# Kernel optimization log

Measured on AMD Instinct MI355X. Metric: run time of the kernel, lower is better.

## Reference

```python
import jax, jax.numpy as jnp
import numpy as np

B, C, H, W = 16, 512, 32, 32
HID = 4 * C


def setup_inputs() -> dict:
    key = jax.random.key(0)
    k_x, k_w1, k_w2 = jax.random.split(key, 3)
    x = jax.random.normal(k_x, (B, C, H, W), dtype=jnp.float32)
    # 1x1 conv weights stored as [out, in] matrices (kernel_size=1)
    w1 = jax.random.normal(k_w1, (HID, C), dtype=jnp.float32) * (1.0 / np.sqrt(C))
    b1 = jnp.zeros((HID,), dtype=jnp.float32)
    w2 = jax.random.normal(k_w2, (C, HID), dtype=jnp.float32) * (1.0 / np.sqrt(HID))
    b2 = jnp.zeros((C,), dtype=jnp.float32)
    return {"x": x, "w1": w1, "b1": b1, "w2": w2, "b2": b2}


def reference(x, w1, b1, w2, b2):
    Bd, Cd, Hd, Wd = x.shape
    scale = Cd ** (-0.5)
    xf = x.reshape(Bd, Cd, Hd * Wd)          # [B, C, N]
    q = jnp.swapaxes(xf, -1, -2)              # [B, N, C]
    # full spatial self-attention: scores [B, N, N]
    attn = jax.nn.softmax(jnp.einsum('bnc,bcm->bnm', q, xf) * scale, axis=-1)
    out = jnp.einsum('bnm,bmc->bnc', attn, q)  # [B, N, C]
    # 1x1-conv FFN applied per spatial position
    h = jax.nn.relu(jnp.einsum('bnc,dc->bnd', out, w1) + b1)   # [B, N, 4C]
    y = jnp.einsum('bnd,cd->bnc', h, w2) + b2                  # [B, N, C]
    y = jnp.swapaxes(y, -1, -2).reshape(Bd, Cd, Hd, Wd)
    return y + x
```

## Files before the change

### kernel.cpp

```cpp
#include <hip/hip_runtime.h>

#define BATCH 16
#define CH    512
#define NSP   1024
#define HIDD  2048

typedef __bf16 bf16x8 __attribute__((ext_vector_type(8)));
typedef float floatx4 __attribute__((ext_vector_type(4)));

__device__ __forceinline__ float bf2f(unsigned short u) {
    union { unsigned int i; float f; } v; v.i = ((unsigned int)u) << 16; return v.f;
}
__device__ __forceinline__ unsigned short f2bf(float f) {
    union { float f; unsigned int i; } v; v.f = f;
    unsigned int i = v.i;
    return (unsigned short)((i + 0x7FFFu + ((i >> 16) & 1u)) >> 16);
}

__device__ __forceinline__ void gload16(const void* g, void* l) {
    __builtin_amdgcn_global_load_lds(
        (__attribute__((address_space(1))) unsigned int*)(g),
        (__attribute__((address_space(3))) unsigned int*)(l),
        16, 0, 0);
}
#define MEMFENCE asm volatile("" ::: "memory")

template<int EPI, int MAP, int DEPTH>
__global__ __launch_bounds__(256, (DEPTH == 2) ? 3 : 2)
void gemm_bt(const unsigned short* __restrict__ A,
             const unsigned short* __restrict__ Bm,
             void* __restrict__ Cout,
             int Nn, int K,
             long sAb, long sBb, long sCb,
             const float* __restrict__ bias, float scale,
             const float* __restrict__ resid,
             float* __restrict__ aux)
{
    constexpr int NBUF = DEPTH + 1;
    __shared__ unsigned short sA[NBUF][128 * 32];
    __shared__ unsigned short sB[NBUF][128 * 32];

    const int tid  = threadIdx.x;
    const int lane = tid & 63;
    const int w    = tid >> 6;
    const int quad = lane >> 4;
    const int l15  = lane & 15;
    const int mw   = (w >> 1) * 64;
    const int nw   = (w & 1) * 64;

    const int F = blockIdx.x;
    int m0, n0, b;
    if constexpr (MAP == 0) {
        const int xcd = F & 7, s = F >> 3;
        b = xcd + ((s >> 6) << 3);
        const int j = s & 63; m0 = (j >> 3) << 7; n0 = (j & 7) << 7;
    } else if constexpr (MAP == 1) {
        const int xcd = F & 7, s = F >> 3;
        b = xcd + ((s >> 5) << 3);
        const int j = s & 31; m0 = (j >> 2) << 7; n0 = (j & 3) << 7;
    } else if constexpr (MAP == 2) {
        b = 0; m0 = (F >> 4) << 7; n0 = (F & 15) << 7;
    } else {
        const int xcd = F & 7, s = F >> 3;
        b = 0; m0 = (s & 3) << 7; n0 = ((xcd << 4) + (s >> 2)) << 7;
    }

    A  += (size_t)b * sAb;
    Bm += (size_t)b * sBb;

    const int srow = lane >> 2;
    const int sg   = (lane & 3) ^ ((lane >> 3) & 3);
    const unsigned short* pA = A  + (size_t)(m0 + w * 32 + srow) * K + sg * 8;
    const unsigned short* pB = Bm + (size_t)(n0 + w * 32 + srow) * K + sg * 8;
    const size_t rowskip16 = (size_t)16 * K;
    const int woff = w * 1024;
    const int rslot = ((l15 >> 1) & 3);

    floatx4 acc[4][4];
#pragma unroll
    for (int i = 0; i < 4; i++)
#pragma unroll
        for (int j = 0; j < 4; j++) acc[i][j] = (floatx4){0.f, 0.f, 0.f, 0.f};

    const int nIter = K >> 5;
    const int kLast = K - 32;

#pragma unroll
    for (int d = 0; d < DEPTH; ++d) {
        unsigned short* dA = &sA[d][0] + woff;
        unsigned short* dB = &sB[d][0] + woff;
        gload16(pA + d * 32,             dA);
        gload16(pA + d * 32 + rowskip16, dA + 512);
        gload16(pB + d * 32,             dB);
        gload16(pB + d * 32 + rowskip16, dB + 512);
        MEMFENCE;
    }

    int bcur = 0, bpf = DEPTH;
    for (int it = 0; it < nIter; ++it) {
        if constexpr (DEPTH == 2)
            asm volatile("s_waitcnt vmcnt(4)\n\ts_barrier" ::: "memory");
        else
            asm volatile("s_waitcnt vmcnt(8)\n\ts_barrier" ::: "memory");

        const int kpf = (it + DEPTH) * 32 <= kLast ? (it + DEPTH) * 32 : kLast;
        unsigned short* dA = &sA[0][0] + bpf * 4096 + woff;
        unsigned short* dB = &sB[0][0] + bpf * 4096 + woff;
        gload16(pA + kpf,             dA);
        gload16(pA + kpf + rowskip16, dA + 512);
        gload16(pB + kpf,             dB);
        gload16(pB + kpf + rowskip16, dB + 512);
        MEMFENCE;

        const unsigned short* bufA = &sA[0][0] + bcur * 4096;
        const unsigned short* bufB = &sB[0][0] + bcur * 4096;
        bf16x8 af[4], bfr[4];
#pragma unroll
        for (int mi = 0; mi < 4; mi++)
            af[mi] = *(const bf16x8*)(bufA + (mw + mi * 16 + l15) * 32
                                      + (quad ^ rslot) * 8);
#pragma unroll
        for (int ni = 0; ni < 4; ni++)
            bfr[ni] = *(const bf16x8*)(bufB + (nw + ni * 16 + l15) * 32
                                       + (quad ^ rslot) * 8);
#pragma unroll
        for (int mi = 0; mi < 4; mi++)
#pragma unroll
            for (int ni = 0; ni < 4; ni++)
                acc[mi][ni] = __builtin_amdgcn_mfma_f32_16x16x32_bf16(
                    af[mi], bfr[ni], acc[mi][ni], 0, 0, 0);

        bcur = bcur == NBUF - 1 ? 0 : bcur + 1;
        bpf  = bpf  == NBUF - 1 ? 0 : bpf  + 1;
    }
    asm volatile("s_waitcnt vmcnt(0)" ::: "memory");

    if constexpr (EPI == 4) {
        float* Of = (float*)Cout;
#pragma unroll
        for (int mi = 0; mi < 4; mi++) {
#pragma unroll
            for (int r = 0; r < 4; r++) {
                const int c = m0 + mw + mi * 16 + quad * 4 + r;
                const float bv = bias[c];
#pragma unroll
                for (int ni = 0; ni < 4; ni++) {
                    const int j  = n0 + nw + ni * 16 + l15;
                    const int bb = j >> 10, ns = j & 1023;
                    const size_t a = (size_t)bb * CH * NSP + (size_t)c * NSP + ns;
                    Of[a] = acc[mi][ni][r] + bv + resid[a];
                }
            }
        }
    } else if constexpr (EPI == 5) {
#pragma unroll
        for (int mi = 0; mi < 4; mi++)
#pragma unroll
            for (int ni = 0; ni < 4; ni++)
#pragma unroll
                for (int r = 0; r < 4; r++)
                    acc[mi][ni][r] = __expf(acc[mi][ni][r] * scale);
        {
            const int chunk = (n0 + nw) >> 6;
            float* ps = aux + (size_t)b * NSP * 16;
#pragma unroll
            for (int mi = 0; mi < 4; mi++) {
#pragma unroll
                for (int r = 0; r < 4; r++) {
                    float s = acc[mi][0][r] + acc[mi][1][r]
                            + acc[mi][2][r] + acc[mi][3][r];
                    s += __shfl_xor(s, 1);
                    s += __shfl_xor(s, 2);
                    s += __shfl_xor(s, 4);
                    s += __shfl_xor(s, 8);
                    if (l15 == 0)
                        ps[(size_t)(m0 + mw + mi * 16 + quad * 4 + r) * 16
                           + chunk] = s;
                }
            }
        }
        unsigned short* Cb = (unsigned short*)Cout + (size_t)b * sCb;
#pragma unroll
        for (int mi = 0; mi < 4; mi++) {
#pragma unroll
            for (int r = 0; r < 4; r++) {
                const size_t rowoff =
                    (size_t)(m0 + mw + mi * 16 + quad * 4 + r) * Nn;
#pragma unroll
                for (int ni = 0; ni < 4; ni++)
                    Cb[rowoff + n0 + nw + ni * 16 + l15] =
                        f2bf(acc[mi][ni][r]);
            }
        }
    } else if constexpr (EPI == 6) {
        const float* invp = aux + (size_t)b * NSP;
        unsigned short* Cb = (unsigned short*)Cout + (size_t)b * sCb;
#pragma unroll
        for (int mi = 0; mi < 4; mi++) {
#pragma unroll
            for (int r = 0; r < 4; r++) {
                const int row = m0 + mw + mi * 16 + quad * 4 + r;
                const float iv = invp[row];
                const size_t rowoff = (size_t)row * Nn;
#pragma unroll
                for (int ni = 0; ni < 4; ni++)
                    Cb[rowoff + n0 + nw + ni * 16 + l15] =
                        f2bf(acc[mi][ni][r] * iv);
            }
        }
    } else {
        unsigned short* Cb = (unsigned short*)Cout + (size_t)b * sCb;
        float bv[4];
#pragma unroll
        for (int ni = 0; ni < 4; ni++) bv[ni] = bias[n0 + nw + ni * 16 + l15];
#pragma unroll
        for (int mi = 0; mi < 4; mi++) {
#pragma unroll
            for (int r = 0; r < 4; r++) {
                const size_t rowoff =
                    (size_t)(m0 + mw + mi * 16 + quad * 4 + r) * Nn;
#pragma unroll
                for (int ni = 0; ni < 4; ni++)
                    Cb[rowoff + n0 + nw + ni * 16 + l15] =
                        f2bf(fmaxf(acc[mi][ni][r] + bv[ni], 0.f));
            }
        }
    }
}

__global__ __launch_bounds__(256)
void rowsum_inv_kernel(const float* __restrict__ ps, float* __restrict__ inv)
{
    const int i = blockIdx.x * 256 + threadIdx.x;
    const float* p = ps + (size_t)i * 16;
    float s = 0.f;
#pragma unroll
    for (int k = 0; k < 16; k++) s += p[k];
    inv[i] = 1.0f / s;
}

__global__ __launch_bounds__(256)
void pack_x_kernel(const float* __restrict__ x,
                   unsigned short* __restrict__ Xbf,
                   unsigned short* __restrict__ XT)
{
    __shared__ float tile[32][33];
    const int tx = threadIdx.x, ty = threadIdx.y;
    const int n0 = blockIdx.x * 32, c0 = blockIdx.y * 32, b = blockIdx.z;
    const size_t base = (size_t)b * CH * NSP;
#pragma unroll
    for (int i = ty; i < 32; i += 8) {
        float v = x[base + (size_t)(c0 + i) * NSP + n0 + tx];
        tile[i][tx] = v;
        Xbf[base + (size_t)(c0 + i) * NSP + n0 + tx] = f2bf(v);
    }
    __syncthreads();
    const size_t tbase = (size_t)b * NSP * CH;
#pragma unroll
    for (int i = ty; i < 32; i += 8)
        XT[tbase + (size_t)(n0 + i) * CH + c0 + tx] = f2bf(tile[tx][i]);
}

__global__ __launch_bounds__(256)
void cast_bf16_kernel(const float* __restrict__ src,
                      unsigned short* __restrict__ dst, int n)
{
    int i = blockIdx.x * 256 + threadIdx.x;
    if (i < n) dst[i] = f2bf(src[i]);
}

extern "C" void kernel_launch(void* const* d_in, const int* in_sizes, int n_in,
                              void* d_out, int out_size, void* d_ws, size_t ws_size,
                              hipStream_t stream)
{
    const float* x  = (const float*)d_in[0];
    const float* w1 = (const float*)d_in[1];
    const float* b1 = (const float*)d_in[2];
    const float* w2 = (const float*)d_in[3];
    const float* b2 = (const float*)d_in[4];
    float* out = (float*)d_out;

    char* ws = (char*)d_ws;
    unsigned short* Xbf = (unsigned short*)ws; ws += (size_t)BATCH * CH * NSP * 2;
    unsigned short* XT  = (unsigned short*)ws; ws += (size_t)BATCH * NSP * CH * 2;
    unsigned short* W1b = (unsigned short*)ws; ws += (size_t)HIDD * CH * 2;
    unsigned short* W2b = (unsigned short*)ws; ws += (size_t)CH * HIDD * 2;
    unsigned short* P   = (unsigned short*)ws; ws += (size_t)BATCH * NSP * NSP * 2;
    unsigned short* O   = (unsigned short*)ws; ws += (size_t)BATCH * NSP * CH * 2;
    unsigned short* Hb  = (unsigned short*)ws; ws += (size_t)BATCH * NSP * HIDD * 2;
    float*          Ps  = (float*)ws;          ws += (size_t)BATCH * NSP * 16 * 4;
    float*          Inv = (float*)ws;          ws += (size_t)BATCH * NSP * 4;

    const dim3 blk(256);

    pack_x_kernel<<<dim3(NSP / 32, CH / 32, BATCH), dim3(32, 8), 0, stream>>>(x, Xbf, XT);
    cast_bf16_kernel<<<dim3((HIDD * CH) / 256), blk, 0, stream>>>(w1, W1b, HIDD * CH);
    cast_bf16_kernel<<<dim3((CH * HIDD) / 256), blk, 0, stream>>>(w2, W2b, CH * HIDD);

    gemm_bt<5, 0, 2><<<dim3(1024), blk, 0, stream>>>(
        XT, XT, P, NSP, CH,
        (long)NSP * CH, (long)NSP * CH, (long)NSP * NSP, nullptr,
        0.04419417382415922f, nullptr, Ps);

    rowsum_inv_kernel<<<dim3(BATCH * NSP / 256), blk, 0, stream>>>(Ps, Inv);

    gemm_bt<6, 1, 2><<<dim3(512), blk, 0, stream>>>(
        P, Xbf, O, CH, NSP,
        (long)NSP * NSP, (long)CH * NSP, (long)NSP * CH, nullptr, 1.f,
        nullptr, Inv);

    gemm_bt<2, 2, 3><<<dim3(2048), blk, 0, stream>>>(
        O, W1b, Hb, HIDD, CH, 0, 0, 0, b1, 1.f, nullptr, nullptr);

    gemm_bt<4, 3, 3><<<dim3(512), blk, 0, stream>>>(
        W2b, Hb, out, BATCH * NSP, HIDD, 0, 0, 0, b2, 1.f, x, nullptr);
}
```

Measured before the change: 277.8 us.

## Exploit score matrix symmetry: compute upper-triangle tiles and mirror-write transposes

The X^T X score GEMM is symmetric, so the grid is reduced to upper-triangular 128x128 tiles per batch (36 per batch) and each off-diagonal tile also writes its transposed copy and the matching partial row sums. This cuts the matmul work for the score stage nearly in half at the cost of a second, transposed store pass and an uneven tile mapping. The FFN1 GEMM pipeline depth is also lowered from 3 to 2. It relies on the exponent of a symmetric score remaining symmetric, which holds here because the stabilisation is not row-dependent.

```diff
diff --git a/kernel.cpp b/kernel.cpp
--- a/kernel.cpp
+++ b/kernel.cpp
@@ -50,19 +50,22 @@
 
     const int F = blockIdx.x;
     int m0, n0, b;
-    if constexpr (MAP == 0) {
-        const int xcd = F & 7, s = F >> 3;
-        b = xcd + ((s >> 6) << 3);
-        const int j = s & 63; m0 = (j >> 3) << 7; n0 = (j & 7) << 7;
-    } else if constexpr (MAP == 1) {
+    if constexpr (MAP == 1) {
         const int xcd = F & 7, s = F >> 3;
         b = xcd + ((s >> 5) << 3);
         const int j = s & 31; m0 = (j >> 2) << 7; n0 = (j & 3) << 7;
     } else if constexpr (MAP == 2) {
         b = 0; m0 = (F >> 4) << 7; n0 = (F & 15) << 7;
-    } else {
+    } else if constexpr (MAP == 3) {
         const int xcd = F & 7, s = F >> 3;
         b = 0; m0 = (s & 3) << 7; n0 = ((xcd << 4) + (s >> 2)) << 7;
+    } else {
+        const int xcd = F & 7; int s = F >> 3;
+        b = xcd + ((s >= 36) ? 8 : 0);
+        if (s >= 36) s -= 36;
+        int tm = 0;
+        while (s >= 8 - tm) { s -= 8 - tm; tm++; }
+        m0 = tm << 7; n0 = (tm + s) << 7;
     }
 
     A  += (size_t)b * sAb;
@@ -192,6 +195,39 @@
                         f2bf(acc[mi][ni][r]);
             }
         }
+        if constexpr (MAP == 4) {
+            if (m0 != n0) {
+                const int chunkt = (m0 + mw) >> 6;
+                float* ps = aux + (size_t)b * NSP * 16;
+#pragma unroll
+                for (int ni = 0; ni < 4; ni++) {
+                    float s = 0.f;
+#pragma unroll
+                    for (int mi = 0; mi < 4; mi++)
+#pragma unroll
+                        for (int r = 0; r < 4; r++) s += acc[mi][ni][r];
+                    s += __shfl_xor(s, 16);
+                    s += __shfl_xor(s, 32);
+                    if (quad == 0)
+                        ps[(size_t)(n0 + nw + ni * 16 + l15) * 16 + chunkt] = s;
+                }
+#pragma unroll
+                for (int ni = 0; ni < 4; ni++) {
+                    const size_t rowoff =
+                        (size_t)(n0 + nw + ni * 16 + l15) * Nn;
+#pragma unroll
+                    for (int mi = 0; mi < 4; mi++) {
+                        ushort4 v;
+                        v.x = f2bf(acc[mi][ni][0]);
+                        v.y = f2bf(acc[mi][ni][1]);
+                        v.z = f2bf(acc[mi][ni][2]);
+                        v.w = f2bf(acc[mi][ni][3]);
+                        *(ushort4*)(Cb + rowoff + m0 + mw + mi * 16 + quad * 4)
+                            = v;
+                    }
+                }
+            }
+        }
     } else if constexpr (EPI == 6) {
         const float* invp = aux + (size_t)b * NSP;
         unsigned short* Cb = (unsigned short*)Cout + (size_t)b * sCb;
@@ -297,7 +333,7 @@
     cast_bf16_kernel<<<dim3((HIDD * CH) / 256), blk, 0, stream>>>(w1, W1b, HIDD * CH);
     cast_bf16_kernel<<<dim3((CH * HIDD) / 256), blk, 0, stream>>>(w2, W2b, CH * HIDD);
 
-    gemm_bt<5, 0, 2><<<dim3(1024), blk, 0, stream>>>(
+    gemm_bt<5, 4, 2><<<dim3(576), blk, 0, stream>>>(
         XT, XT, P, NSP, CH,
         (long)NSP * CH, (long)NSP * CH, (long)NSP * NSP, nullptr,
         0.04419417382415922f, nullptr, Ps);
@@ -309,7 +345,7 @@
         (long)NSP * NSP, (long)CH * NSP, (long)NSP * CH, nullptr, 1.f,
         nullptr, Inv);
 
-    gemm_bt<2, 2, 3><<<dim3(2048), blk, 0, stream>>>(
+    gemm_bt<2, 2, 2><<<dim3(2048), blk, 0, stream>>>(
         O, W1b, Hb, HIDD, CH, 0, 0, 0, b1, 1.f, nullptr, nullptr);
 
     gemm_bt<4, 3, 3><<<dim3(512), blk, 0, stream>>>(
```

Result: faster. 262.7 us (-5.4%).
